# Optimization experiments

Hardware: AMD Instinct MI355X
Metric: run time of the kernel (lower is better)

Reference implementation:

```python
import jax, jax.numpy as jnp
import numpy as np

B, N, D, E, H = 4, 2048, 512, 16, 1024
CAP = max(4, min(N, int(N * 2.0 / E)))   # eval capacity_factor = 2.0 -> 256
EPS = 1e-9
THRESH = 0.2  # second_threshold_eval


def setup_inputs() -> dict:
    key = jax.random.key(0)
    ks = jax.random.split(key, 10)
    f32 = jnp.float32
    return {
        "X": jax.random.normal(ks[0], (B, N, D), f32),
        "probs": jax.random.uniform(ks[1], (B, N), f32),
        "W1": jax.random.normal(ks[2], (D, D), f32) * (1.0 / np.sqrt(D)),
        "b1": jnp.zeros((D,), f32),
        "Wg": jax.random.normal(ks[3], (D, E), f32),  # Top2Gating uses randn init
        "We1": jax.random.normal(ks[4], (E, D, H), f32) * (1.0 / np.sqrt(D)),
        "We2": jax.random.normal(ks[5], (E, H, D), f32) * (1.0 / np.sqrt(H)),
        "W3": jax.random.normal(ks[6], (D, 4), f32) * (1.0 / np.sqrt(D)),
        "b3": jnp.zeros((4,), f32),
        "W4": jax.random.normal(ks[7], (4, 1), f32) * 0.5,
        "b4": jnp.zeros((1,), f32),
    }


def top2_gating(x, Wg, probs):
    # x: [B, N, D] -> raw gates [B, N, E]
    raw = jax.nn.softmax(jnp.einsum('bnd,de->bne', x, Wg), axis=-1)
    dt = raw.dtype

    gate1 = jnp.max(raw, axis=-1)
    idx1 = jnp.argmax(raw, axis=-1)
    mask1 = jax.nn.one_hot(idx1, E, dtype=dt)
    density_proxy = raw

    raw_wo1 = raw * (1.0 - mask1)
    gate2 = jnp.max(raw_wo1, axis=-1)
    idx2 = jnp.argmax(raw_wo1, axis=-1)
    mask2 = jax.nn.one_hot(idx2, E, dtype=dt)

    denom = gate1 + gate2 + EPS
    gate1 = gate1 / denom
    gate2 = gate2 / denom

    # load-balancing loss (computed but wrapper discards it)
    density1 = jnp.mean(mask1, axis=-2)
    loss = jnp.mean(jnp.mean(density_proxy, axis=-2) * density1) * float(E ** 2)

    # second policy == 'random'
    mask2 = mask2 * (probs < (gate2 / max(THRESH, EPS))).astype(dt)[..., None]

    # exclusive cumsum along the group dim gives position within each expert
    pos1 = (jnp.cumsum(mask1, axis=-2) - mask1) * mask1          # [B, N, E]
    mask1 = mask1 * (pos1 < float(CAP)).astype(dt)
    mask1_count = jnp.sum(mask1, axis=-2, keepdims=True)
    mask1_flat = jnp.sum(mask1, axis=-1)                          # [B, N]
    pos1_flat = jnp.sum(pos1, axis=-1)
    gate1 = gate1 * mask1_flat

    pos2 = ((jnp.cumsum(mask2, axis=-2) - mask2) + mask1_count) * mask2
    mask2 = mask2 * (pos2 < float(CAP)).astype(dt)
    mask2_flat = jnp.sum(mask2, axis=-1)
    pos2_flat = jnp.sum(pos2, axis=-1)
    gate2 = gate2 * mask2_flat

    # safe one-hot: out-of-range positions map to all-zeros (jax.nn.one_hot semantics)
    oh_p1 = jax.nn.one_hot(pos1_flat.astype(jnp.int32), CAP, dtype=dt)
    oh_p2 = jax.nn.one_hot(pos2_flat.astype(jnp.int32), CAP, dtype=dt)
    oh_e1 = jax.nn.one_hot(idx1, E, dtype=dt)
    oh_e2 = jax.nn.one_hot(idx2, E, dtype=dt)

    combine = ((gate1 * mask1_flat)[..., None, None] * oh_e1[..., :, None] * oh_p1[..., None, :]
               + (gate2 * mask2_flat)[..., None, None] * oh_e2[..., :, None] * oh_p2[..., None, :])
    dispatch = (combine != 0).astype(dt)
    return dispatch, combine, loss


def reference(X, probs, W1, b1, Wg, We1, We2, W3, b3, W4, b4):
    h = X @ W1 + b1                                              # linear1
    dispatch, combine, loss = top2_gating(h, Wg, probs)
    exp_in = jnp.einsum('bnd,bnec->ebcd', h, dispatch)           # dispatch
    hid = jax.nn.leaky_relu(jnp.einsum('ebcd,edh->ebch', exp_in, We1))
    exp_out = jnp.einsum('ebch,ehd->ebcd', hid, We2)             # experts
    moe_out = jnp.einsum('bnec,ebcd->bnd', combine, exp_out)     # combine
    out = (moe_out @ W3 + b3) @ W4 + b4                          # hidden3 -> act3
    return out
```

## Files before the change

kernel.cpp:

```cpp
#include <hip/hip_runtime.h>
#include <hip/hip_bf16.h>

#define NB 4
#define NN 2048
#define ND 512
#define NE 16
#define NH 1024
#define CAP 256
#define NTOK (NB*NN)

typedef __attribute__((ext_vector_type(8))) short bf16x8;
typedef __attribute__((ext_vector_type(4))) float f32x4;
typedef __attribute__((ext_vector_type(8))) unsigned short u16x8;

__device__ __forceinline__ void gload16(const void* gsrc, void* lds) {
    __builtin_amdgcn_global_load_lds((const __attribute__((address_space(1))) void*)gsrc,
                                     (__attribute__((address_space(3))) void*)lds, 16, 0, 0);
}
__device__ __forceinline__ unsigned short f2bf(float f) {
    union { __hip_bfloat16 b; unsigned short u; } v; v.b = __float2bfloat16(f); return v.u;
}

__global__ __launch_bounds__(256) void prep_kernel(const float* __restrict__ W1,
                                                   const float* __restrict__ Wg,
                                                   unsigned short* __restrict__ W1B,
                                                   float* __restrict__ WcT,
                                                   float* __restrict__ zbuf) {
    const int tid = threadIdx.x;
    int bid = blockIdx.x;
    if (bid < 128) {
        const int w = tid >> 6, l = tid & 63;
        const int d = bid * 4 + w;
        float a0 = 0.f, a1 = 0.f, a2 = 0.f, a3 = 0.f, a4 = 0.f, a5 = 0.f, a6 = 0.f, a7 = 0.f;
        float a8 = 0.f, a9 = 0.f, aA = 0.f, aB = 0.f, aC = 0.f, aD = 0.f, aE = 0.f, aF = 0.f;
        #pragma unroll
        for (int ch = 0; ch < 8; ++ch) {
            float x = W1[(size_t)d * ND + ch * 64 + l];
            const float4* wg4 = (const float4*)(Wg + (size_t)(ch * 64 + l) * NE);
            float4 g0 = wg4[0], g1 = wg4[1], g2 = wg4[2], g3 = wg4[3];
            a0 = fmaf(x, g0.x, a0); a1 = fmaf(x, g0.y, a1); a2 = fmaf(x, g0.z, a2); a3 = fmaf(x, g0.w, a3);
            a4 = fmaf(x, g1.x, a4); a5 = fmaf(x, g1.y, a5); a6 = fmaf(x, g1.z, a6); a7 = fmaf(x, g1.w, a7);
            a8 = fmaf(x, g2.x, a8); a9 = fmaf(x, g2.y, a9); aA = fmaf(x, g2.z, aA); aB = fmaf(x, g2.w, aB);
            aC = fmaf(x, g3.x, aC); aD = fmaf(x, g3.y, aD); aE = fmaf(x, g3.z, aE); aF = fmaf(x, g3.w, aF);
        }
        float accs[16] = {a0, a1, a2, a3, a4, a5, a6, a7, a8, a9, aA, aB, aC, aD, aE, aF};
        #pragma unroll
        for (int off = 32; off >= 1; off >>= 1)
            #pragma unroll
            for (int e = 0; e < 16; ++e) accs[e] += __shfl_xor(accs[e], off);
        #pragma unroll
        for (int e = 0; e < 16; ++e)
            if (l == e) WcT[e * ND + d] = accs[e];
        return;
    }
    bid -= 128;
    {
        if (bid == 0) zbuf[tid] = 0.f;
        int dblk = bid >> 1, hblk = bid & 1;
        const float* src = W1 + (size_t)(dblk * 64) * ND + hblk * 256 + tid;
        unsigned short* dst = W1B + (size_t)(dblk * 512 + hblk * 256 + tid) * 64;
        float v[64];
        #pragma unroll
        for (int j = 0; j < 64; ++j) v[j] = src[(size_t)j * ND];
        #pragma unroll
        for (int q = 0; q < 8; ++q) {
            u16x8 o;
            #pragma unroll
            for (int j = 0; j < 8; ++j) o[j] = f2bf(v[q * 8 + j]);
            *(u16x8*)(dst + q * 8) = o;
        }
    }
}

__global__ __launch_bounds__(256) void gating_kernel(const float* __restrict__ X,
                                                     const float* __restrict__ WcT,
                                                     const float* __restrict__ probs,
                                                     const float* __restrict__ b3,
                                                     const float* __restrict__ W4,
                                                     const float* __restrict__ b4,
                                                     unsigned short* __restrict__ Xbf,
                                                     int* __restrict__ idx1a, int* __restrict__ idx2a,
                                                     float* __restrict__ g1a, float* __restrict__ g2a,
                                                     float* __restrict__ out) {
    __shared__ float wc[NE * ND];
    const int tid = threadIdx.x;
    #pragma unroll
    for (int i = 0; i < 32; ++i) wc[tid + 256 * i] = WcT[tid + 256 * i];
    float c0v = b4[0];
    #pragma unroll
    for (int j = 0; j < 4; ++j) c0v += b3[j] * W4[j];
    __syncthreads();
    const int w = tid >> 6, l = tid & 63;
    const float4* wc4 = (const float4*)wc;
    for (int j = 0; j < 4; ++j) {
        int tok = blockIdx.x * 16 + j * 4 + w;
        const float4* xrow = (const float4*)(X + (size_t)tok * ND);
        float4 x0 = xrow[l], x1 = xrow[l + 64];
        {
            ushort4 o0, o1;
            o0.x = f2bf(x0.x); o0.y = f2bf(x0.y); o0.z = f2bf(x0.z); o0.w = f2bf(x0.w);
            o1.x = f2bf(x1.x); o1.y = f2bf(x1.y); o1.z = f2bf(x1.z); o1.w = f2bf(x1.w);
            *(ushort4*)(Xbf + (size_t)tok * ND + 4 * l) = o0;
            *(ushort4*)(Xbf + (size_t)tok * ND + 256 + 4 * l) = o1;
        }
        float acc[NE];
        #pragma unroll
        for (int e = 0; e < NE; ++e) {
            float4 w0 = wc4[e * 128 + l], w1 = wc4[e * 128 + l + 64];
            acc[e] = x0.x * w0.x + x0.y * w0.y + x0.z * w0.z + x0.w * w0.w
                   + x1.x * w1.x + x1.y * w1.y + x1.z * w1.z + x1.w * w1.w;
        }
        #pragma unroll
        for (int off = 32; off >= 1; off >>= 1)
            #pragma unroll
            for (int e = 0; e < NE; ++e) acc[e] += __shfl_xor(acc[e], off);

        if (l == 0) {
            float m = acc[0];
            #pragma unroll
            for (int e = 1; e < NE; ++e) m = fmaxf(m, acc[e]);
            float raw[NE]; float s = 0.f;
            #pragma unroll
            for (int e = 0; e < NE; ++e) { raw[e] = expf(acc[e] - m); s += raw[e]; }
            #pragma unroll
            for (int e = 0; e < NE; ++e) raw[e] = raw[e] / s;
            int i1 = 0; float g1 = raw[0];
            #pragma unroll
            for (int e = 1; e < NE; ++e) if (raw[e] > g1) { g1 = raw[e]; i1 = e; }
            int i2 = -1; float g2 = -1.f;
            #pragma unroll
            for (int e = 0; e < NE; ++e) if (e != i1 && raw[e] > g2) { g2 = raw[e]; i2 = e; }
            float denom = g1 + g2 + 1e-9f;
            float g1n = g1 / denom, g2n = g2 / denom;
            bool flag = probs[tok] < (g2n / 0.2f);
            idx1a[tok] = i1;
            idx2a[tok] = flag ? i2 : -1;
            g1a[tok] = g1n;
            g2a[tok] = g2n;
            out[tok] = c0v;
        }
    }
}

__global__ __launch_bounds__(512) void scan_linear1_kernel(const int* __restrict__ idx1a,
                                                           const int* __restrict__ idx2a,
                                                           int* __restrict__ slot_token,
                                                           const unsigned short* __restrict__ Xbf,
                                                           const unsigned short* __restrict__ W1B,
                                                           const float* __restrict__ b1,
                                                           unsigned short* __restrict__ hbf,
                                                           const float* __restrict__ We1,
                                                           unsigned short* __restrict__ We1B,
                                                           const float* __restrict__ We2,
                                                           const float* __restrict__ W3,
                                                           const float* __restrict__ W4,
                                                           float* __restrict__ u) {
    __shared__ char smem[65536];
    const int tid = threadIdx.x;
    const int w = tid >> 6, l = tid & 63;
    if (blockIdx.x < 64) {
        const int bb = blockIdx.x;
        const int b = bb >> 4, e = bb & 15;
        int* cnt1 = (int*)smem;
        int* cnt2 = cnt1 + 8;
        int* slot = slot_token + (e * NB + b) * CAP;
        const unsigned long long below = (l == 0) ? 0ull : ((1ull << l) - 1ull);
        const int base0 = w * 256;
        int c1 = 0, c2 = 0;
        #pragma unroll
        for (int it = 0; it < 4; ++it) {
            int n = base0 + it * 64 + l;
            c1 += __popcll(__ballot(idx1a[b * NN + n] == e));
            c2 += __popcll(__ballot(idx2a[b * NN + n] == e));
        }
        if (l == 0) { cnt1[w] = c1; cnt2[w] = c2; }
        __syncthreads();
        int b1c = 0, t1 = 0, b2c = 0, t2 = 0;
        #pragma unroll
        for (int i = 0; i < 8; ++i) {
            int v1 = cnt1[i], v2 = cnt2[i];
            if (i < w) { b1c += v1; b2c += v2; }
            t1 += v1; t2 += v2;
        }
        const int start2 = (t1 < CAP) ? t1 : CAP;
        int c = b1c;
        #pragma unroll
        for (int it = 0; it < 4; ++it) {
            int n = base0 + it * 64 + l;
            bool p = (idx1a[b * NN + n] == e);
            unsigned long long m = __ballot(p);
            int pre = __popcll(m & below);
            if (p) { int pos = c + pre; if (pos < CAP) slot[pos] = n; }
            c += __popcll(m);
        }
        c = start2 + b2c;
        #pragma unroll
        for (int it = 0; it < 4; ++it) {
            int n = base0 + it * 64 + l;
            bool p = (idx2a[b * NN + n] == e);
            unsigned long long m = __ballot(p);
            int pre = __popcll(m & below);
            if (p) { int pos = c + pre; if (pos < CAP) slot[pos] = n | (1 << 30); }
            c += __popcll(m);
        }
        int nfill = start2 + t2; nfill = (nfill < CAP) ? nfill : CAP;
        for (int i = nfill + tid; i < CAP; i += 512) slot[i] = -1;
        return;
    }
    if (blockIdx.x < 320) {
        const int lb = blockIdx.x - 64;
        const int m0 = (lb >> 2) * 128, n0 = (lb & 3) * 128;
        const int wm = w >> 1, wn = w & 1;
        const int lr = l & 15, lk = l >> 4;
        char* Ash0 = smem;
        char* Bsh0 = smem + 32768;

        auto stage = [&](int Ks, int buf) {
            #pragma unroll
            for (int i = 0; i < 2; ++i) {
                int o = i * 8192 + tid * 16;
                int r = o >> 7, bb = o & 127;
                int sb = bb ^ ((r & 7) << 4);
                gload16((const char*)Xbf + ((size_t)(m0 + r) * ND + Ks * 64) * 2 + sb,
                        Ash0 + buf * 16384 + i * 8192 + w * 1024);
                gload16((const char*)W1B + ((size_t)(Ks * 512 + n0 + r) * 64) * 2 + sb,
                        Bsh0 + buf * 16384 + i * 8192 + w * 1024);
            }
        };

        f32x4 acc[2][4] = {};
        stage(0, 0);
        __syncthreads();
        for (int Ks = 0; Ks < 8; ++Ks) {
            int buf = Ks & 1;
            if (Ks < 7) stage(Ks + 1, buf ^ 1);
            #pragma unroll
            for (int k32 = 0; k32 < 2; ++k32) {
                int kb = (k32 * 32 + 8 * lk) * 2;
                bf16x8 a[2], bfr[4];
                #pragma unroll
                for (int mi = 0; mi < 2; ++mi) {
                    int row = wm * 32 + mi * 16 + lr;
                    a[mi] = *(const bf16x8*)(Ash0 + buf * 16384 + row * 128 + (kb ^ ((row & 7) << 4)));
                }
                #pragma unroll
                for (int ni = 0; ni < 4; ++ni) {
                    int row = wn * 64 + ni * 16 + lr;
                    bfr[ni] = *(const bf16x8*)(Bsh0 + buf * 16384 + row * 128 + (kb ^ ((row & 7) << 4)));
                }
                #pragma unroll
                for (int mi = 0; mi < 2; ++mi)
                    #pragma unroll
                    for (int ni = 0; ni < 4; ++ni)
                        acc[mi][ni] = __builtin_amdgcn_mfma_f32_16x16x32_bf16(a[mi], bfr[ni], acc[mi][ni], 0, 0, 0);
            }
            __syncthreads();
        }
        #pragma unroll
        for (int mi = 0; mi < 2; ++mi)
            #pragma unroll
            for (int ni = 0; ni < 4; ++ni) {
                int col = n0 + wn * 64 + ni * 16 + lr;
                float bb1 = b1[col];
                #pragma unroll
                for (int r = 0; r < 4; ++r) {
                    int m = m0 + wm * 32 + mi * 16 + lk * 4 + r;
                    hbf[(size_t)m * ND + col] = f2bf(acc[mi][ni][r] + bb1);
                }
            }
        return;
    }
    if (blockIdx.x < 448) {
        const int tb = blockIdx.x - 320;
        #pragma unroll
        for (int q2 = 0; q2 < 2; ++q2) {
            const int unit = tb * 2 + q2;
            const int e = unit >> 4, rem = unit & 15;
            const int dblk = rem >> 1, hblk2 = rem & 1;
            const float* src = We1 + (size_t)e * ND * NH + (size_t)(dblk * 64) * NH + hblk2 * 512 + tid;
            unsigned short* dst = We1B + ((size_t)(e * 8 + dblk) * NH + hblk2 * 512 + tid) * 64;
            float v[64];
            #pragma unroll
            for (int j = 0; j < 64; ++j) v[j] = src[(size_t)j * NH];
            #pragma unroll
            for (int q = 0; q < 8; ++q) {
                u16x8 o;
                #pragma unroll
                for (int j = 0; j < 8; ++j) o[j] = f2bf(v[q * 8 + j]);
                *(u16x8*)(dst + q * 8) = o;
            }
        }
        return;
    }
    {
        const int ub = blockIdx.x - 448;
        float* vvs = (float*)smem;
        {
            int d = tid;
            float s0 = 0.f;
            #pragma unroll
            for (int j = 0; j < 4; ++j) s0 += W3[d * 4 + j] * W4[j];
            vvs[d] = s0;
        }
        __syncthreads();
        const float4* vv4 = (const float4*)vvs;
        const float4 v0 = vv4[l], v1 = vv4[l + 64];
        #pragma unroll
        for (int pass = 0; pass < 2; ++pass) {
            float sums[8];
            #pragma unroll
            for (int i = 0; i < 8; ++i) {
                int gr = ub * 128 + pass * 64 + w * 8 + i;
                const float4* row = (const float4*)(We2 + (size_t)gr * ND);
                float4 a0 = row[l], a1 = row[l + 64];
                sums[i] = a0.x * v0.x + a0.y * v0.y + a0.z * v0.z + a0.w * v0.w
                        + a1.x * v1.x + a1.y * v1.y + a1.z * v1.z + a1.w * v1.w;
            }
            #pragma unroll
            for (int off = 32; off >= 1; off >>= 1)
                #pragma unroll
                for (int i = 0; i < 8; ++i) sums[i] += __shfl_xor(sums[i], off);
            if (l == 0) {
                int gr0 = ub * 128 + pass * 64 + w * 8;
                #pragma unroll
                for (int i = 0; i < 8; ++i) u[gr0 + i] = sums[i];
            }
        }
    }
}

__global__ __launch_bounds__(512) void expert_mfma_kernel(const unsigned short* __restrict__ hbf,
                                                          const unsigned short* __restrict__ We1B,
                                                          const float* __restrict__ u,
                                                          const int* __restrict__ slot_token,
                                                          const float* __restrict__ zbuf,
                                                          const float* __restrict__ g1a,
                                                          const float* __restrict__ g2a,
                                                          float* __restrict__ out) {
    __shared__ char Ash[65536];
    __shared__ char Bsh[2][32768];
    __shared__ float u_lds[NH];
    __shared__ float sbuf[8][64];
    __shared__ int toks[64];
    const int tid = threadIdx.x;
    const int w = tid >> 6, l = tid & 63;
    const int lr = l & 15, lk = l >> 4;
    const int bid = blockIdx.x;
    const int e = (bid & 7) | ((bid >> 7) << 3);
    const int chunk = (bid >> 3) & 15;
    const int b = chunk >> 2, c0 = (chunk & 3) * 64;

    if (tid < 64) toks[tid] = slot_token[(e * NB + b) * CAP + c0 + tid];
    u_lds[tid] = u[e * NH + tid];
    u_lds[tid + 512] = u[e * NH + tid + 512];
    __syncthreads();
    #pragma unroll
    for (int i = 0; i < 8; ++i) {
        int r = i * 8 + w;
        int t = toks[r];
        int tok = t & 2047;
        int sb = (l * 16) ^ ((r & 7) << 4);
        const char* src = (t >= 0) ? ((const char*)hbf + ((size_t)(b * NN + tok) * ND) * 2 + sb)
                                   : ((const char*)zbuf + sb);
        gload16(src, Ash + i * 8192 + w * 1024);
    }
    auto stageB = [&](int s, int buf) {
        int Hc = s >> 4, Ks = s & 15;
        const size_t base = ((size_t)(e * 8 + (Ks >> 1)) * NH + Hc * 512) * 64 + (Ks & 1) * 32;
        #pragma unroll
        for (int i = 0; i < 4; ++i) {
            int r = i * 128 + w * 16 + (l >> 2);
            int swzr = ((r >> 1) & 3) << 4;
            int ebyte = ((l & 3) * 16) ^ swzr;
            gload16((const char*)We1B + (base + (size_t)r * 64) * 2 + ebyte,
                    Bsh[buf] + i * 8192 + w * 1024);
        }
    };
    f32x4 acc[4][4] = {};
    float srow[4][4] = {};
    stageB(0, 0);
    __syncthreads();
    for (int s = 0; s < 32; ++s) {
        int buf = s & 1;
        if (s < 31) stageB(s + 1, buf ^ 1);
        int Ks = s & 15;
        bf16x8 a[4], bb[4];
        #pragma unroll
        for (int mi = 0; mi < 4; ++mi) {
            int row = mi * 16 + lr;
            int kb = (Ks * 64 + lk * 16) ^ ((row & 7) << 4);
            a[mi] = *(const bf16x8*)(Ash + row * 1024 + kb);
        }
        #pragma unroll
        for (int ni = 0; ni < 4; ++ni) {
            int row = w * 64 + ni * 16 + lr;
            int kb = (lk * 16) ^ (((row >> 1) & 3) << 4);
            bb[ni] = *(const bf16x8*)(Bsh[buf] + row * 64 + kb);
        }
        #pragma unroll
        for (int mi = 0; mi < 4; ++mi)
            #pragma unroll
            for (int ni = 0; ni < 4; ++ni)
                acc[mi][ni] = __builtin_amdgcn_mfma_f32_16x16x32_bf16(a[mi], bb[ni], acc[mi][ni], 0, 0, 0);
        if ((s & 15) == 15) {
            int Hc = s >> 4;
            #pragma unroll
            for (int ni = 0; ni < 4; ++ni) {
                float uu = u_lds[Hc * 512 + w * 64 + ni * 16 + lr];
                #pragma unroll
                for (int mi = 0; mi < 4; ++mi)
                    #pragma unroll
                    for (int r = 0; r < 4; ++r) {
                        float x = acc[mi][ni][r];
                        x = (x > 0.f) ? x : 0.01f * x;
                        srow[mi][r] = fmaf(x, uu, srow[mi][r]);
                        acc[mi][ni][r] = 0.f;
                    }
            }
        }
        __syncthreads();
    }
    #pragma unroll
    for (int off = 1; off < 16; off <<= 1)
        #pragma unroll
        for (int mi = 0; mi < 4; ++mi)
            #pragma unroll
            for (int r = 0; r < 4; ++r)
                srow[mi][r] += __shfl_xor(srow[mi][r], off);
    if (lr == 0) {
        #pragma unroll
        for (int mi = 0; mi < 4; ++mi)
            #pragma unroll
            for (int r = 0; r < 4; ++r)
                sbuf[w][mi * 16 + lk * 4 + r] = srow[mi][r];
    }
    __syncthreads();
    if (tid < 64) {
        float s = 0.f;
        #pragma unroll
        for (int q = 0; q < 8; ++q) s += sbuf[q][tid];
        int v = toks[tid];
        if (v >= 0) {
            int tok = v & 2047;
            float g = (v & (1 << 30)) ? g2a[b * NN + tok] : g1a[b * NN + tok];
            atomicAdd(out + b * NN + tok, s * g);
        }
    }
}

extern "C" void kernel_launch(void* const* d_in, const int* in_sizes, int n_in,
                              void* d_out, int out_size, void* d_ws, size_t ws_size,
                              hipStream_t stream) {
    const float* X    = (const float*)d_in[0];
    const float* probs= (const float*)d_in[1];
    const float* W1   = (const float*)d_in[2];
    const float* b1   = (const float*)d_in[3];
    const float* Wg   = (const float*)d_in[4];
    const float* We1  = (const float*)d_in[5];
    const float* We2  = (const float*)d_in[6];
    const float* W3   = (const float*)d_in[7];
    const float* b3   = (const float*)d_in[8];
    const float* W4   = (const float*)d_in[9];
    const float* b4   = (const float*)d_in[10];
    float* out = (float*)d_out;

    char* ws = (char*)d_ws;
    size_t off = 0;
    auto alloc = [&](size_t bytes) { void* p = ws + off; off += (bytes + 255) & ~(size_t)255; return p; };
    unsigned short* Xbf  = (unsigned short*)alloc((size_t)NTOK * ND * 2);
    unsigned short* hbf  = (unsigned short*)alloc((size_t)NTOK * ND * 2);
    unsigned short* W1B  = (unsigned short*)alloc((size_t)ND * ND * 2);
    unsigned short* We1B = (unsigned short*)alloc((size_t)NE * NH * ND * 2);
    float* WcT     = (float*)alloc(NE * ND * 4);
    float* u       = (float*)alloc(NE * NH * 4);
    float* zbuf    = (float*)alloc(1024);
    int*   idx1a   = (int*)alloc(NTOK * 4);
    int*   idx2a   = (int*)alloc(NTOK * 4);
    float* g1a     = (float*)alloc(NTOK * 4);
    float* g2a     = (float*)alloc(NTOK * 4);
    int*   slot_tok= (int*)alloc(NE * NB * CAP * 4);
    (void)ws_size; (void)in_sizes; (void)n_in; (void)out_size;

    prep_kernel<<<144, 256, 0, stream>>>(W1, Wg, W1B, WcT, zbuf);
    gating_kernel<<<NTOK / 16, 256, 0, stream>>>(X, WcT, probs, b3, W4, b4, Xbf,
                                                 idx1a, idx2a, g1a, g2a, out);
    scan_linear1_kernel<<<576, 512, 0, stream>>>(idx1a, idx2a, slot_tok,
                                                 Xbf, W1B, b1, hbf,
                                                 We1, We1B, We2, W3, W4, u);
    expert_mfma_kernel<<<256, 512, 0, stream>>>(hbf, We1B, u, slot_tok, zbuf, g1a, g2a, out);
}
```

Baseline: 84.48 us.

## Move We1 bf16 conversion and We2 projection into the first prep kernel

The We1 transpose/bf16 conversion and the u = We2·(W3·W4) projection move out of the scan/linear1 kernel into the initial prep kernel, which grows from 144 to 912 blocks. These weight-only jobs then run before the gating kernel instead of sharing a launch with the token-dependent scan and linear1 GEMM, leaving scan_linear1 with 320 blocks. The We1 conversion now uses 256-thread blocks, one unit each, and the We2 projection uses 256-thread blocks. The aim is to shorten the critical path of the later kernels, at the cost of making the prep launch, which gating waits on, much larger.

```diff
diff --git a/kernel.cpp b/kernel.cpp
--- a/kernel.cpp
+++ b/kernel.cpp
@@ -21,11 +21,17 @@
     union { __hip_bfloat16 b; unsigned short u; } v; v.b = __float2bfloat16(f); return v.u;
 }
 
-__global__ __launch_bounds__(256) void prep_kernel(const float* __restrict__ W1,
-                                                   const float* __restrict__ Wg,
-                                                   unsigned short* __restrict__ W1B,
-                                                   float* __restrict__ WcT,
-                                                   float* __restrict__ zbuf) {
+__global__ __launch_bounds__(256) void prep_stream_kernel(const float* __restrict__ W1,
+                                                          const float* __restrict__ Wg,
+                                                          const float* __restrict__ We1,
+                                                          const float* __restrict__ We2,
+                                                          const float* __restrict__ W3,
+                                                          const float* __restrict__ W4,
+                                                          unsigned short* __restrict__ W1B,
+                                                          unsigned short* __restrict__ We1B,
+                                                          float* __restrict__ WcT,
+                                                          float* __restrict__ u,
+                                                          float* __restrict__ zbuf) {
     const int tid = threadIdx.x;
     int bid = blockIdx.x;
     if (bid < 128) {
@@ -54,7 +60,7 @@
         return;
     }
     bid -= 128;
-    {
+    if (bid < 16) {
         if (bid == 0) zbuf[tid] = 0.f;
         int dblk = bid >> 1, hblk = bid & 1;
         const float* src = W1 + (size_t)(dblk * 64) * ND + hblk * 256 + tid;
@@ -68,6 +74,64 @@
             #pragma unroll
             for (int j = 0; j < 8; ++j) o[j] = f2bf(v[q * 8 + j]);
             *(u16x8*)(dst + q * 8) = o;
+        }
+        return;
+    }
+    bid -= 16;
+    if (bid < 512) {
+        const int e = bid >> 5, rem = bid & 31;
+        const int dblk = rem >> 2, hq = rem & 3;
+        const float* src = We1 + (size_t)e * ND * NH + (size_t)(dblk * 64) * NH + hq * 256 + tid;
+        unsigned short* dst = We1B + ((size_t)(e * 8 + dblk) * NH + hq * 256 + tid) * 64;
+        float v[64];
+        #pragma unroll
+        for (int j = 0; j < 64; ++j) v[j] = src[(size_t)j * NH];
+        #pragma unroll
+        for (int q = 0; q < 8; ++q) {
+            u16x8 o;
+            #pragma unroll
+            for (int j = 0; j < 8; ++j) o[j] = f2bf(v[q * 8 + j]);
+            *(u16x8*)(dst + q * 8) = o;
+        }
+        return;
+    }
+    bid -= 512;
+    {
+        __shared__ float vvs[ND];
+        {
+            int d = tid * 2;
+            float s0 = 0.f, s1 = 0.f;
+            #pragma unroll
+            for (int j = 0; j < 4; ++j) {
+                s0 += W3[d * 4 + j] * W4[j];
+                s1 += W3[(d + 1) * 4 + j] * W4[j];
+            }
+            vvs[d] = s0; vvs[d + 1] = s1;
+        }
+        __syncthreads();
+        const int w = tid >> 6, l = tid & 63;
+        const float4* vv4 = (const float4*)vvs;
+        const float4 v0 = vv4[l], v1 = vv4[l + 64];
+        #pragma unroll
+        for (int pass = 0; pass < 2; ++pass) {
+            float sums[8];
+            #pragma unroll
+            for (int i = 0; i < 8; ++i) {
+                int gr = bid * 64 + pass * 32 + w * 8 + i;
+                const float4* row = (const float4*)(We2 + (size_t)gr * ND);
+                float4 a0 = row[l], a1 = row[l + 64];
+                sums[i] = a0.x * v0.x + a0.y * v0.y + a0.z * v0.z + a0.w * v0.w
+                        + a1.x * v1.x + a1.y * v1.y + a1.z * v1.z + a1.w * v1.w;
+            }
+            #pragma unroll
+            for (int off = 32; off >= 1; off >>= 1)
+                #pragma unroll
+                for (int i = 0; i < 8; ++i) sums[i] += __shfl_xor(sums[i], off);
+            if (l == 0) {
+                int gr0 = bid * 64 + pass * 32 + w * 8;
+                #pragma unroll
+                for (int i = 0; i < 8; ++i) u[gr0 + i] = sums[i];
+            }
         }
     }
 }
@@ -148,13 +212,7 @@
                                                            const unsigned short* __restrict__ Xbf,
                                                            const unsigned short* __restrict__ W1B,
                                                            const float* __restrict__ b1,
-                                                           unsigned short* __restrict__ hbf,
-                                                           const float* __restrict__ We1,
-                                                           unsigned short* __restrict__ We1B,
-                                                           const float* __restrict__ We2,
-                                                           const float* __restrict__ W3,
-                                                           const float* __restrict__ W4,
-                                                           float* __restrict__ u) {
+                                                           unsigned short* __restrict__ hbf) {
     __shared__ char smem[65536];
     const int tid = threadIdx.x;
     const int w = tid >> 6, l = tid & 63;
@@ -207,126 +265,66 @@
         for (int i = nfill + tid; i < CAP; i += 512) slot[i] = -1;
         return;
     }
-    if (blockIdx.x < 320) {
-        const int lb = blockIdx.x - 64;
-        const int m0 = (lb >> 2) * 128, n0 = (lb & 3) * 128;
-        const int wm = w >> 1, wn = w & 1;
-        const int lr = l & 15, lk = l >> 4;
-        char* Ash0 = smem;
-        char* Bsh0 = smem + 32768;
-
-        auto stage = [&](int Ks, int buf) {
-            #pragma unroll
-            for (int i = 0; i < 2; ++i) {
-                int o = i * 8192 + tid * 16;
-                int r = o >> 7, bb = o & 127;
-                int sb = bb ^ ((r & 7) << 4);
-                gload16((const char*)Xbf + ((size_t)(m0 + r) * ND + Ks * 64) * 2 + sb,
-                        Ash0 + buf * 16384 + i * 8192 + w * 1024);
-                gload16((const char*)W1B + ((size_t)(Ks * 512 + n0 + r) * 64) * 2 + sb,
-                        Bsh0 + buf * 16384 + i * 8192 + w * 1024);
-            }
-        };
-
-        f32x4 acc[2][4] = {};
-        stage(0, 0);
+    const int lb = blockIdx.x - 64;
+    const int m0 = (lb >> 2) * 128, n0 = (lb & 3) * 128;
+    const int wm = w >> 1, wn = w & 1;
+    const int lr = l & 15, lk = l >> 4;
+    char* Ash0 = smem;
+    char* Bsh0 = smem + 32768;
+
+    auto stage = [&](int Ks, int buf) {
+        #pragma unroll
+        for (int i = 0; i < 2; ++i) {
+            int o = i * 8192 + tid * 16;
+            int r = o >> 7, bb = o & 127;
+            int sb = bb ^ ((r & 7) << 4);
+            gload16((const char*)Xbf + ((size_t)(m0 + r) * ND + Ks * 64) * 2 + sb,
+                    Ash0 + buf * 16384 + i * 8192 + w * 1024);
+            gload16((const char*)W1B + ((size_t)(Ks * 512 + n0 + r) * 64) * 2 + sb,
+                    Bsh0 + buf * 16384 + i * 8192 + w * 1024);
+        }
+    };
+
+    f32x4 acc[2][4] = {};
+    stage(0, 0);
+    __syncthreads();
+    for (int Ks = 0; Ks < 8; ++Ks) {
+        int buf = Ks & 1;
+        if (Ks < 7) stage(Ks + 1, buf ^ 1);
+        #pragma unroll
+        for (int k32 = 0; k32 < 2; ++k32) {
+            int kb = (k32 * 32 + 8 * lk) * 2;
+            bf16x8 a[2], bfr[4];
+            #pragma unroll
+            for (int mi = 0; mi < 2; ++mi) {
+                int row = wm * 32 + mi * 16 + lr;
+                a[mi] = *(const bf16x8*)(Ash0 + buf * 16384 + row * 128 + (kb ^ ((row & 7) << 4)));
+            }
+            #pragma unroll
+            for (int ni = 0; ni < 4; ++ni) {
+                int row = wn * 64 + ni * 16 + lr;
+                bfr[ni] = *(const bf16x8*)(Bsh0 + buf * 16384 + row * 128 + (kb ^ ((row & 7) << 4)));
+            }
+            #pragma unroll
+            for (int mi = 0; mi < 2; ++mi)
+                #pragma unroll
+                for (int ni = 0; ni < 4; ++ni)
+                    acc[mi][ni] = __builtin_amdgcn_mfma_f32_16x16x32_bf16(a[mi], bfr[ni], acc[mi][ni], 0, 0, 0);
+        }
         __syncthreads();
-        for (int Ks = 0; Ks < 8; ++Ks) {
-            int buf = Ks & 1;
-            if (Ks < 7) stage(Ks + 1, buf ^ 1);
-            #pragma unroll
-            for (int k32 = 0; k32 < 2; ++k32) {
-                int kb = (k32 * 32 + 8 * lk) * 2;
-                bf16x8 a[2], bfr[4];
-                #pragma unroll
-                for (int mi = 0; mi < 2; ++mi) {
-                    int row = wm * 32 + mi * 16 + lr;
-                    a[mi] = *(const bf16x8*)(Ash0 + buf * 16384 + row * 128 + (kb ^ ((row & 7) << 4)));
-                }
-                #pragma unroll
-                for (int ni = 0; ni < 4; ++ni) {
-                    int row = wn * 64 + ni * 16 + lr;
-                    bfr[ni] = *(const bf16x8*)(Bsh0 + buf * 16384 + row * 128 + (kb ^ ((row & 7) << 4)));
-                }
-                #pragma unroll
-                for (int mi = 0; mi < 2; ++mi)
-                    #pragma unroll
-                    for (int ni = 0; ni < 4; ++ni)
-                        acc[mi][ni] = __builtin_amdgcn_mfma_f32_16x16x32_bf16(a[mi], bfr[ni], acc[mi][ni], 0, 0, 0);
-            }
-            __syncthreads();
-        }
-        #pragma unroll
-        for (int mi = 0; mi < 2; ++mi)
-            #pragma unroll
-            for (int ni = 0; ni < 4; ++ni) {
-                int col = n0 + wn * 64 + ni * 16 + lr;
-                float bb1 = b1[col];
-                #pragma unroll
-                for (int r = 0; r < 4; ++r) {
-                    int m = m0 + wm * 32 + mi * 16 + lk * 4 + r;
-                    hbf[(size_t)m * ND + col] = f2bf(acc[mi][ni][r] + bb1);
-                }
-            }
-        return;
-    }
-    if (blockIdx.x < 448) {
-        const int tb = blockIdx.x - 320;
-        #pragma unroll
-        for (int q2 = 0; q2 < 2; ++q2) {
-            const int unit = tb * 2 + q2;
-            const int e = unit >> 4, rem = unit & 15;
-            const int dblk = rem >> 1, hblk2 = rem & 1;
-            const float* src = We1 + (size_t)e * ND * NH + (size_t)(dblk * 64) * NH + hblk2 * 512 + tid;
-            unsigned short* dst = We1B + ((size_t)(e * 8 + dblk) * NH + hblk2 * 512 + tid) * 64;
-            float v[64];
-            #pragma unroll
-            for (int j = 0; j < 64; ++j) v[j] = src[(size_t)j * NH];
-            #pragma unroll
-            for (int q = 0; q < 8; ++q) {
-                u16x8 o;
-                #pragma unroll
-                for (int j = 0; j < 8; ++j) o[j] = f2bf(v[q * 8 + j]);
-                *(u16x8*)(dst + q * 8) = o;
-            }
-        }
-        return;
-    }
-    {
-        const int ub = blockIdx.x - 448;
-        float* vvs = (float*)smem;
-        {
-            int d = tid;
-            float s0 = 0.f;
-            #pragma unroll
-            for (int j = 0; j < 4; ++j) s0 += W3[d * 4 + j] * W4[j];
-            vvs[d] = s0;
-        }
-        __syncthreads();
-        const float4* vv4 = (const float4*)vvs;
-        const float4 v0 = vv4[l], v1 = vv4[l + 64];
-        #pragma unroll
-        for (int pass = 0; pass < 2; ++pass) {
-            float sums[8];
-            #pragma unroll
-            for (int i = 0; i < 8; ++i) {
-                int gr = ub * 128 + pass * 64 + w * 8 + i;
-                const float4* row = (const float4*)(We2 + (size_t)gr * ND);
-                float4 a0 = row[l], a1 = row[l + 64];
-                sums[i] = a0.x * v0.x + a0.y * v0.y + a0.z * v0.z + a0.w * v0.w
-                        + a1.x * v1.x + a1.y * v1.y + a1.z * v1.z + a1.w * v1.w;
-            }
-            #pragma unroll
-            for (int off = 32; off >= 1; off >>= 1)
-                #pragma unroll
-                for (int i = 0; i < 8; ++i) sums[i] += __shfl_xor(sums[i], off);
-            if (l == 0) {
-                int gr0 = ub * 128 + pass * 64 + w * 8;
-                #pragma unroll
-                for (int i = 0; i < 8; ++i) u[gr0 + i] = sums[i];
-            }
-        }
-    }
+    }
+    #pragma unroll
+    for (int mi = 0; mi < 2; ++mi)
+        #pragma unroll
+        for (int ni = 0; ni < 4; ++ni) {
+            int col = n0 + wn * 64 + ni * 16 + lr;
+            float bb1 = b1[col];
+            #pragma unroll
+            for (int r = 0; r < 4; ++r) {
+                int m = m0 + wm * 32 + mi * 16 + lk * 4 + r;
+                hbf[(size_t)m * ND + col] = f2bf(acc[mi][ni][r] + bb1);
+            }
+        }
 }
 
 __global__ __launch_bounds__(512) void expert_mfma_kernel(const unsigned short* __restrict__ hbf,
@@ -481,11 +479,11 @@
     int*   slot_tok= (int*)alloc(NE * NB * CAP * 4);
     (void)ws_size; (void)in_sizes; (void)n_in; (void)out_size;
 
-    prep_kernel<<<144, 256, 0, stream>>>(W1, Wg, W1B, WcT, zbuf);
+    prep_stream_kernel<<<912, 256, 0, stream>>>(W1, Wg, We1, We2, W3, W4,
+                                                W1B, We1B, WcT, u, zbuf);
     gating_kernel<<<NTOK / 16, 256, 0, stream>>>(X, WcT, probs, b3, W4, b4, Xbf,
                                                  idx1a, idx2a, g1a, g2a, out);
-    scan_linear1_kernel<<<576, 512, 0, stream>>>(idx1a, idx2a, slot_tok,
-                                                 Xbf, W1B, b1, hbf,
-                                                 We1, We1B, We2, W3, W4, u);
+    scan_linear1_kernel<<<320, 512, 0, stream>>>(idx1a, idx2a, slot_tok,
+                                                 Xbf, W1B, b1, hbf);
     expert_mfma_kernel<<<256, 512, 0, stream>>>(hbf, We1B, u, slot_tok, zbuf, g1a, g2a, out);
 }
```

New measurement: 83.76 us. Within noise of the previous version (-0.9%).
